# Performance work log

Hardware: AMD Instinct MI355X
Metric: run time of the kernel (lower is better)

The kernel has to match this reference:

```python
import jax, jax.numpy as jnp
import numpy as np
from math import ceil, log2

LEVELS = 6
N = 4096
DB4 = np.array([0.23037781330885523, 0.7148465705525415, 0.6308807679295904,
                -0.02798376941698385, -0.18703481171888114, 0.030841381835986965,
                0.032883011666982945, -0.010597401784997278], dtype=np.float32)


def setup_inputs() -> dict:
    key = jax.random.key(0)
    x = jax.random.normal(key, (N, N), dtype=jnp.float32)
    # learned filter bank: scaling.repeat(levels*2, 1)
    scaling = jnp.tile(jnp.asarray(DB4), (LEVELS * 2, 1))
    return {
        "x": x,
        "scaling": scaling,
        "alpha": jnp.float32(10.0),
        "b_plus": jnp.float32(2.0),
        "b_minus": jnp.float32(1.0),
    }


def compute_wavelet(h):
    # g_k = flip(h); odd indices negated
    g = jnp.flip(h, -1)
    sign = jnp.where(jnp.arange(g.shape[-1]) % 2 == 1, -1.0, 1.0).astype(g.dtype)
    return g * sign


def convolve(x, f, transpose=False):
    # circular convolution (or correlation if transpose) along last axis via FFT,
    # exactly as torch rfft/irfft with n=input_length
    L = x.shape[-1]
    fa = jnp.fft.rfft(x, axis=-1)
    fb = jnp.fft.rfft(f, n=L)
    if transpose:
        fb = jnp.conj(fb)
    return jnp.fft.irfft(fa * fb, n=L, axis=-1)


def forward_layer(x, h):
    w = compute_wavelet(h)
    return convolve(x, w)[:, ::2], convolve(x, h)[:, ::2]


def backward_layer(d, a, h):
    w = compute_wavelet(h)
    fd = jnp.zeros((d.shape[0], d.shape[1] * 2), d.dtype).at[:, ::2].set(d)
    fa = jnp.zeros((a.shape[0], a.shape[1] * 2), a.dtype).at[:, ::2].set(a)
    return convolve(fd, w, transpose=True) + convolve(fa, h, transpose=True)


def forward2d(x, hH, hV):
    d, a = forward_layer(x, hH)
    hh, hl = forward_layer(d.T, hV)
    hh, hl = hh.T, hl.T
    lh, ll = forward_layer(a.T, hV)
    lh, ll = lh.T, ll.T
    return (hh, hl, lh), ll


def backward2d(hh, hl, lh, ll, hH, hV):
    h = backward_layer(hh.T, hl.T, hV).T
    l = backward_layer(lh.T, ll.T, hV).T
    return backward_layer(h, l, hH)


def _despawn(x, scaling, alpha, b_plus, b_minus):
    n, m = x.shape
    pn = 2 ** ceil(log2(n)) - n
    pm = 2 ** ceil(log2(m)) - m
    xp = jnp.pad(x, ((0, pn), (0, pm)), mode="edge") if (pn or pm) else x

    approx = xp
    coeffs = []
    for lev in range(LEVELS):
        dets, approx = forward2d(approx, scaling[lev], scaling[lev + 1])
        coeffs.append(dets)

    def thr(t):
        return t * (jax.nn.sigmoid(alpha * (t - b_plus)) + jax.nn.sigmoid(-alpha * (t + b_minus)))

    filt = [tuple(thr(c) for c in tup) for tup in coeffs] + [thr(approx)]

    a = filt[-1]
    for lev in reversed(range(LEVELS)):
        hh, hl, lh = filt[lev]
        a = backward2d(hh, hl, lh, a, scaling[lev], scaling[lev + 1])

    flat = jnp.concatenate(
        [jnp.concatenate(tup, axis=-1).reshape(-1) for tup in filt[:-1]]
        + [filt[-1].reshape(-1)]
    )
    return a[:n, :m], flat


def reference(x, scaling, alpha, b_plus, b_minus):
    return _despawn(x, scaling, alpha, b_plus, b_minus)
```

## Files before the change

kernel.cpp:

```cpp
#include <hip/hip_runtime.h>


#define CORE_WGS 64

__device__ __forceinline__ float thrf(float t, float alpha, float bp, float bm) {
    float s1 = 1.0f / (1.0f + __expf(-alpha * (t - bp)));
    float s2 = 1.0f / (1.0f + __expf( alpha * (t + bm)));
    return t * (s1 + s2);
}

__device__ __forceinline__ void load_filt(const float* __restrict__ filt,
                                          float (&h)[8], float (&w)[8]) {
#pragma unroll
    for (int k = 0; k < 8; ++k) h[k] = filt[k];
#pragma unroll
    for (int k = 0; k < 8; ++k) w[k] = (k & 1) ? -h[7 - k] : h[7 - k];
}

struct SMemF {
    float xs[70][72];
    float Ds[70][36];
    float As[70][36];
};
struct SMemI {
    float hh[36][36], hl[36][36], lh[36][36], as0[36][36];
    float Hs[64][36], Ls[64][36];
};
union SMem {
    SMemF f;
    SMemI i;
};

__device__ __forceinline__ void gbar(unsigned* bar, unsigned k, unsigned nwg, int tid) {
    __syncthreads();
    if (tid == 0) {
        __threadfence();
        unsigned old = atomicAdd(&bar[0], 1u);
        if (old == k * nwg - 1u) {
            __hip_atomic_store(&bar[1], k, __ATOMIC_RELEASE, __HIP_MEMORY_SCOPE_AGENT);
            (void)__hip_atomic_load(&bar[1], __ATOMIC_ACQUIRE, __HIP_MEMORY_SCOPE_AGENT);
        } else {
            unsigned g;
            do {
                __builtin_amdgcn_s_sleep(2);
                g = __hip_atomic_load(&bar[1], __ATOMIC_ACQUIRE, __HIP_MEMORY_SCOPE_AGENT);
            } while (g < k);
        }
    }
    __syncthreads();
}

__device__ __forceinline__ void fwd_tile(
    SMemF& sm, const float* __restrict__ X, int s, int sh,
    float* __restrict__ flat, float* __restrict__ All, bool thr_ll,
    const float (&hr)[8], const float (&wr)[8],
    const float (&hc)[8], const float (&wc)[8],
    float alpha, float bp, float bm, int i0, int j0, int tid) {
    const int smk = s - 1;
    for (int idx = tid; idx < 70 * 18; idx += 256) {
        int rr = idx / 18, c = idx - rr * 18;
        int gr = (2 * i0 - 7 + rr) & smk;
        int gc = (2 * j0 - 8 + 4 * c) & smk;
        *(float4*)&sm.xs[rr][4 * c] = *(const float4*)&X[(size_t)gr * s + gc];
    }
    __syncthreads();
    for (int idx = tid; idx < 70 * 8; idx += 256) {
        int rr = idx >> 3, q = idx & 7;
        const float4* xr = (const float4*)&sm.xs[rr][8 * q];
        float wv[16];
#pragma unroll
        for (int m = 0; m < 4; ++m) {
            float4 t = xr[m];
            wv[4 * m + 0] = t.x; wv[4 * m + 1] = t.y;
            wv[4 * m + 2] = t.z; wv[4 * m + 3] = t.w;
        }
        float d[4], a[4];
#pragma unroll
        for (int e = 0; e < 4; ++e) {
            float dd = 0.f, aa = 0.f;
#pragma unroll
            for (int u = 0; u < 8; ++u) {
                float v = wv[2 * e + 1 + u];
                dd += wr[7 - u] * v;
                aa += hr[7 - u] * v;
            }
            d[e] = dd; a[e] = aa;
        }
        *(float4*)&sm.Ds[rr][4 * q] = make_float4(d[0], d[1], d[2], d[3]);
        *(float4*)&sm.As[rr][4 * q] = make_float4(a[0], a[1], a[2], a[3]);
    }
    __syncthreads();
    {
        const int j = tid & 31, iq = tid >> 5;
        float Dw[14], Aw[14];
#pragma unroll
        for (int t = 0; t < 14; ++t) {
            Dw[t] = sm.Ds[8 * iq + t][j];
            Aw[t] = sm.As[8 * iq + t][j];
        }
#pragma unroll
        for (int e = 0; e < 4; ++e) {
            float hh = 0.f, hl = 0.f, lh = 0.f, ll = 0.f;
#pragma unroll
            for (int u = 0; u < 8; ++u) {
                float dv = Dw[2 * e + u], av = Aw[2 * e + u];
                hh += wc[7 - u] * dv;
                hl += hc[7 - u] * dv;
                lh += wc[7 - u] * av;
                ll += hc[7 - u] * av;
            }
            int row = i0 + 4 * iq + e;
            size_t ro = (size_t)row * (3 * sh) + (j0 + j);
            flat[ro]          = thrf(hh, alpha, bp, bm);
            flat[ro + sh]     = thrf(hl, alpha, bp, bm);
            flat[ro + 2 * sh] = thrf(lh, alpha, bp, bm);
            All[(size_t)row * sh + (j0 + j)] =
                thr_ll ? thrf(ll, alpha, bp, bm) : ll;
        }
    }
}

__device__ __forceinline__ void inv_tile(
    SMemI& sm, const float* __restrict__ flatl, const float* __restrict__ a,
    int astride, int sc, float* __restrict__ outp, int ostride,
    const float (&hr)[8], const float (&wr)[8],
    const float (&hc)[8], const float (&wc)[8],
    int i0, int m0, int tid) {
    const int mm = sc - 1;
    const int r0 = i0 >> 1, c0 = m0 >> 1;
    const int ds = 3 * sc;
    for (int idx = tid; idx < 4 * 324; idx += 256) {
        int aid = idx / 324, rem = idx - aid * 324;
        int rr = rem / 9, c = rem - rr * 9;
        int gr = (r0 + rr) & mm;
        int gc = (c0 + 4 * c) & mm;
        if (aid == 0)
            *(float4*)&sm.hh[rr][4 * c] = *(const float4*)&flatl[(size_t)gr * ds + gc];
        else if (aid == 1)
            *(float4*)&sm.hl[rr][4 * c] = *(const float4*)&flatl[(size_t)gr * ds + sc + gc];
        else if (aid == 2)
            *(float4*)&sm.lh[rr][4 * c] = *(const float4*)&flatl[(size_t)gr * ds + 2 * sc + gc];
        else
            *(float4*)&sm.as0[rr][4 * c] = *(const float4*)&a[(size_t)gr * astride + gc];
    }
    __syncthreads();
    for (int idx = tid; idx < 16 * 36; idx += 256) {
        int q = idx / 36, jj = idx - q * 36;
        float hv[6], lv[6], gv[6], av[6];
#pragma unroll
        for (int d = 0; d < 6; ++d) {
            int lr = 2 * q + d;
            hv[d] = sm.hh[lr][jj];
            lv[d] = sm.hl[lr][jj];
            gv[d] = sm.lh[lr][jj];
            av[d] = sm.as0[lr][jj];
        }
        float H0 = 0.f, H1 = 0.f, H2 = 0.f, H3 = 0.f;
        float L0 = 0.f, L1 = 0.f, L2 = 0.f, L3 = 0.f;
#pragma unroll
        for (int t = 0; t < 4; ++t) {
            float we = wc[2 * t], he = hc[2 * t];
            float wo = wc[2 * t + 1], ho = hc[2 * t + 1];
            H0 += we * hv[t]     + he * lv[t];
            H1 += wo * hv[t + 1] + ho * lv[t + 1];
            H2 += we * hv[t + 1] + he * lv[t + 1];
            H3 += wo * hv[t + 2] + ho * lv[t + 2];
            L0 += we * gv[t]     + he * av[t];
            L1 += wo * gv[t + 1] + ho * av[t + 1];
            L2 += we * gv[t + 1] + he * av[t + 1];
            L3 += wo * gv[t + 2] + ho * av[t + 2];
        }
        sm.Hs[4 * q + 0][jj] = H0; sm.Hs[4 * q + 1][jj] = H1;
        sm.Hs[4 * q + 2][jj] = H2; sm.Hs[4 * q + 3][jj] = H3;
        sm.Ls[4 * q + 0][jj] = L0; sm.Ls[4 * q + 1][jj] = L1;
        sm.Ls[4 * q + 2][jj] = L2; sm.Ls[4 * q + 3][jj] = L3;
    }
    __syncthreads();
    for (int idx = tid; idx < 64 * 16; idx += 256) {
        int i = idx >> 4, p = idx & 15;
        const float2* hp = (const float2*)&sm.Hs[i][2 * p];
        const float2* lp = (const float2*)&sm.Ls[i][2 * p];
        float2 hA = hp[0], hB = hp[1], hC = hp[2];
        float2 lA = lp[0], lB = lp[1], lC = lp[2];
        float Hw[6] = {hA.x, hA.y, hB.x, hB.y, hC.x, hC.y};
        float Lw[6] = {lA.x, lA.y, lB.x, lB.y, lC.x, lC.y};
        float o0 = 0.f, o1 = 0.f, o2 = 0.f, o3 = 0.f;
#pragma unroll
        for (int t = 0; t < 4; ++t) {
            float we = wr[2 * t], he = hr[2 * t];
            float wo = wr[2 * t + 1], ho = hr[2 * t + 1];
            o0 += we * Hw[t]     + he * Lw[t];
            o1 += wo * Hw[t + 1] + ho * Lw[t + 1];
            o2 += we * Hw[t + 1] + he * Lw[t + 1];
            o3 += wo * Hw[t + 2] + ho * Lw[t + 2];
        }
        *(float4*)&outp[(size_t)(i0 + i) * ostride + (m0 + 4 * p)] =
            make_float4(o0, o1, o2, o3);
    }
}

__global__ __launch_bounds__(256) void fwd_fused(
    const float* __restrict__ X, int s, int sh,
    float* __restrict__ flat, float* __restrict__ All,
    const float* __restrict__ filt_row, const float* __restrict__ filt_col,
    const float* __restrict__ ap, const float* __restrict__ bpp,
    const float* __restrict__ bmp, unsigned* bar_reset) {
    __shared__ SMem smem;
    float hr[8], wr[8], hc[8], wc[8];
    load_filt(filt_row, hr, wr);
    load_filt(filt_col, hc, wc);
    const float alpha = *ap, bp = *bpp, bm = *bmp;
    fwd_tile(smem.f, X, s, sh, flat, All, false, hr, wr, hc, wc,
             alpha, bp, bm, blockIdx.y * 32, blockIdx.x * 32, threadIdx.x);
    if (bar_reset && blockIdx.x == 0 && blockIdx.y == 0 && threadIdx.x == 0) {
        bar_reset[0] = 0u;
        bar_reset[1] = 0u;
    }
}

__global__ __launch_bounds__(256) void inv_fused(
    const float* __restrict__ flatl, const float* __restrict__ a, int astride,
    int sc, float* __restrict__ outp, int ostride,
    const float* __restrict__ filt_col, const float* __restrict__ filt_row) {
    __shared__ SMem smem;
    float hr[8], wr[8], hc[8], wc[8];
    load_filt(filt_row, hr, wr);
    load_filt(filt_col, hc, wc);
    inv_tile(smem.i, flatl, a, astride, sc, outp, ostride, hr, wr, hc, wc,
             blockIdx.y * 64, blockIdx.x * 64, threadIdx.x);
}

__global__ __launch_bounds__(256) void core_small(
    const float* __restrict__ scal, const float* __restrict__ ap,
    const float* __restrict__ bpp, const float* __restrict__ bmp,
    float* __restrict__ out, float* __restrict__ ws, unsigned* bar) {
    __shared__ SMem smem;
    const int tid = threadIdx.x, bid = blockIdx.x, nb = gridDim.x;
    const float alpha = *ap, bp = *bpp, bm = *bmp;
    const int N = 4096;
    float* flat = out + 16777216;
    const size_t Aoff[7]    = {0, 0, 4194304, 5242880, 5505024, 5570560, 5586944};
    const size_t flatOff[6] = {0, 12582912, 15728640, 16515072, 16711680, 16760832};
    const size_t finalOff = 16773120;
    float* P0 = ws + 5591040;
    float* P1 = ws + 5591040 + 4194304;

    unsigned k = 1;
    for (int lev = 3; lev <= 5; ++lev) {
        int s = N >> lev, sh = s >> 1;
        float hr[8], wr[8], hc[8], wc[8];
        load_filt(scal + lev * 8, hr, wr);
        load_filt(scal + (lev + 1) * 8, hc, wc);
        const float* src = ws + Aoff[lev];
        float* All = (lev < 5) ? (ws + Aoff[lev + 1]) : (flat + finalOff);
        int nt = sh >> 5;
        for (int t = bid; t < nt * nt; t += nb)
            fwd_tile(smem.f, src, s, sh, flat + flatOff[lev], All, lev == 5,
                     hr, wr, hc, wc, alpha, bp, bm, (t / nt) * 32, (t % nt) * 32, tid);
        gbar(bar, k++, (unsigned)nb, tid);
    }
    const float* a_in = flat + finalOff;
    for (int lev = 5; lev >= 3; --lev) {
        int sc = N >> (lev + 1), r = 2 * sc;
        float hr[8], wr[8], hc[8], wc[8];
        load_filt(scal + lev * 8, hr, wr);
        load_filt(scal + (lev + 1) * 8, hc, wc);
        float* outp = (lev & 1) ? P1 : P0;
        int nt = r >> 6;
        for (int t = bid; t < nt * nt; t += nb)
            inv_tile(smem.i, flat + flatOff[lev], a_in, sc, sc, outp, r,
                     hr, wr, hc, wc, (t / nt) * 64, (t % nt) * 64, tid);
        a_in = outp;
        if (lev > 3) gbar(bar, k++, (unsigned)nb, tid);
    }
}

extern "C" void kernel_launch(void* const* d_in, const int* in_sizes, int n_in,
                              void* d_out, int out_size, void* d_ws, size_t ws_size,
                              hipStream_t stream) {
    const float* x    = (const float*)d_in[0];
    const float* scal = (const float*)d_in[1];
    const float* ap   = (const float*)d_in[2];
    const float* bp   = (const float*)d_in[3];
    const float* bm   = (const float*)d_in[4];
    float* out = (float*)d_out;
    float* ws  = (float*)d_ws;

    const int N = 4096;
    float* recon = out;
    float* flat  = out + 16777216;
    static const size_t Aoff[7]    = {0, 0, 4194304, 5242880, 5505024, 5570560, 5586944};
    static const size_t flatOff[6] = {0, 12582912, 15728640, 16515072, 16711680, 16760832};
    float* P0 = ws + 5591040;
    float* P1 = ws + 5591040 + 4194304;
    unsigned* bar = (unsigned*)(ws + 14680064);

    dim3 blk(256);

    const float* src = x;
    for (int lev = 0; lev < 3; ++lev) {
        int s = N >> lev, sh = s >> 1;
        dim3 g(sh / 32, sh / 32);
        fwd_fused<<<g, blk, 0, stream>>>(src, s, sh, flat + flatOff[lev],
                                         ws + Aoff[lev + 1],
                                         scal + lev * 8, scal + (lev + 1) * 8,
                                         ap, bp, bm,
                                         (lev == 2) ? bar : (unsigned*)nullptr);
        src = ws + Aoff[lev + 1];
    }

    {
        void* args[] = {(void*)&scal, (void*)&ap, (void*)&bp, (void*)&bm,
                        (void*)&out, (void*)&ws, (void*)&bar};
        hipLaunchCooperativeKernel(core_small, dim3(CORE_WGS), blk, args, 0, stream);
    }

    const float* a_in = P1;
    for (int lev = 2; lev >= 0; --lev) {
        int sc = N >> (lev + 1), r = 2 * sc;
        float* outp = (lev == 0) ? recon : ((lev & 1) ? P1 : P0);
        dim3 g(r / 64, r / 64);
        inv_fused<<<g, blk, 0, stream>>>(flat + flatOff[lev], a_in, sc,
                                         sc, outp, r,
                                         scal + (lev + 1) * 8, scal + lev * 8);
        a_in = outp;
    }
}
```

Baseline: 349.4 us.

## Replace grid barrier with per-phase tile counters and launch core kernel normally

The persistent core kernel's generic grid barrier is replaced by per-phase completion counters, each on its own padded cache line. A block waits only until the previous phase's tile count is reached, and blocks with no tiles skip signalling. The cooperative launch is replaced by a plain launch to cut launch overhead. This relies on all 64 workgroups being co-resident without the cooperative guarantee, and adds extra __syncthreads between tiles in each loop.

```diff
diff --git a/kernel.cpp b/kernel.cpp
--- a/kernel.cpp
+++ b/kernel.cpp
@@ -30,25 +30,6 @@
     SMemF f;
     SMemI i;
 };
-
-__device__ __forceinline__ void gbar(unsigned* bar, unsigned k, unsigned nwg, int tid) {
-    __syncthreads();
-    if (tid == 0) {
-        __threadfence();
-        unsigned old = atomicAdd(&bar[0], 1u);
-        if (old == k * nwg - 1u) {
-            __hip_atomic_store(&bar[1], k, __ATOMIC_RELEASE, __HIP_MEMORY_SCOPE_AGENT);
-            (void)__hip_atomic_load(&bar[1], __ATOMIC_ACQUIRE, __HIP_MEMORY_SCOPE_AGENT);
-        } else {
-            unsigned g;
-            do {
-                __builtin_amdgcn_s_sleep(2);
-                g = __hip_atomic_load(&bar[1], __ATOMIC_ACQUIRE, __HIP_MEMORY_SCOPE_AGENT);
-            } while (g < k);
-        }
-    }
-    __syncthreads();
-}
 
 __device__ __forceinline__ void fwd_tile(
     SMemF& sm, const float* __restrict__ X, int s, int sh,
@@ -212,10 +193,8 @@
     const float alpha = *ap, bp = *bpp, bm = *bmp;
     fwd_tile(smem.f, X, s, sh, flat, All, false, hr, wr, hc, wc,
              alpha, bp, bm, blockIdx.y * 32, blockIdx.x * 32, threadIdx.x);
-    if (bar_reset && blockIdx.x == 0 && blockIdx.y == 0 && threadIdx.x == 0) {
-        bar_reset[0] = 0u;
-        bar_reset[1] = 0u;
-    }
+    if (bar_reset && blockIdx.x == 0 && blockIdx.y == 0 && threadIdx.x < 8)
+        bar_reset[threadIdx.x * 32] = 0u;
 }
 
 __global__ __launch_bounds__(256) void inv_fused(
@@ -233,7 +212,7 @@
 __global__ __launch_bounds__(256) void core_small(
     const float* __restrict__ scal, const float* __restrict__ ap,
     const float* __restrict__ bpp, const float* __restrict__ bmp,
-    float* __restrict__ out, float* __restrict__ ws, unsigned* bar) {
+    float* __restrict__ out, float* __restrict__ ws, unsigned* __restrict__ bar) {
     __shared__ SMem smem;
     const int tid = threadIdx.x, bid = blockIdx.x, nb = gridDim.x;
     const float alpha = *ap, bp = *bpp, bm = *bmp;
@@ -245,33 +224,59 @@
     float* P0 = ws + 5591040;
     float* P1 = ws + 5591040 + 4194304;
 
-    unsigned k = 1;
-    for (int lev = 3; lev <= 5; ++lev) {
-        int s = N >> lev, sh = s >> 1;
+    const float* a_in = flat + finalOff;
+    for (int p = 0; p < 6; ++p) {
+        const int lev = (p < 3) ? (3 + p) : (8 - p);
+        const int nt  = N >> (lev + 6);
+        const int Np  = nt * nt;
+
+        if (p > 0) {
+            const int pl  = (p - 1 < 3) ? (2 + p) : (9 - p);
+            const int pnt = N >> (pl + 6);
+            const unsigned tgt = (unsigned)(pnt * pnt);
+            if (tid == 0) {
+                while (__hip_atomic_load(&bar[(p - 1) * 32], __ATOMIC_RELAXED,
+                                         __HIP_MEMORY_SCOPE_AGENT) < tgt) {
+                    __builtin_amdgcn_s_sleep(2);
+                }
+            }
+            __syncthreads();
+            __builtin_amdgcn_fence(__ATOMIC_ACQUIRE, "agent");
+        }
+
         float hr[8], wr[8], hc[8], wc[8];
         load_filt(scal + lev * 8, hr, wr);
         load_filt(scal + (lev + 1) * 8, hc, wc);
-        const float* src = ws + Aoff[lev];
-        float* All = (lev < 5) ? (ws + Aoff[lev + 1]) : (flat + finalOff);
-        int nt = sh >> 5;
-        for (int t = bid; t < nt * nt; t += nb)
-            fwd_tile(smem.f, src, s, sh, flat + flatOff[lev], All, lev == 5,
-                     hr, wr, hc, wc, alpha, bp, bm, (t / nt) * 32, (t % nt) * 32, tid);
-        gbar(bar, k++, (unsigned)nb, tid);
-    }
-    const float* a_in = flat + finalOff;
-    for (int lev = 5; lev >= 3; --lev) {
-        int sc = N >> (lev + 1), r = 2 * sc;
-        float hr[8], wr[8], hc[8], wc[8];
-        load_filt(scal + lev * 8, hr, wr);
-        load_filt(scal + (lev + 1) * 8, hc, wc);
-        float* outp = (lev & 1) ? P1 : P0;
-        int nt = r >> 6;
-        for (int t = bid; t < nt * nt; t += nb)
-            inv_tile(smem.i, flat + flatOff[lev], a_in, sc, sc, outp, r,
-                     hr, wr, hc, wc, (t / nt) * 64, (t % nt) * 64, tid);
-        a_in = outp;
-        if (lev > 3) gbar(bar, k++, (unsigned)nb, tid);
+        unsigned cnt = 0;
+
+        if (p < 3) {
+            const int s = N >> lev, sh = s >> 1;
+            const float* src = ws + Aoff[lev];
+            float* All = (lev < 5) ? (ws + Aoff[lev + 1]) : (flat + finalOff);
+            for (int t = bid; t < Np; t += nb) {
+                if (cnt) __syncthreads();
+                fwd_tile(smem.f, src, s, sh, flat + flatOff[lev], All, lev == 5,
+                         hr, wr, hc, wc, alpha, bp, bm,
+                         (t / nt) * 32, (t % nt) * 32, tid);
+                ++cnt;
+            }
+        } else {
+            const int sc = N >> (lev + 1), r = 2 * sc;
+            float* outp = (lev & 1) ? P1 : P0;
+            for (int t = bid; t < Np; t += nb) {
+                if (cnt) __syncthreads();
+                inv_tile(smem.i, flat + flatOff[lev], a_in, sc, sc, outp, r,
+                         hr, wr, hc, wc, (t / nt) * 64, (t % nt) * 64, tid);
+                ++cnt;
+            }
+            a_in = outp;
+        }
+
+        __syncthreads();
+        if (tid == 0 && cnt) {
+            __threadfence();
+            atomicAdd(&bar[p * 32], cnt);
+        }
     }
 }
 
@@ -309,11 +314,7 @@
         src = ws + Aoff[lev + 1];
     }
 
-    {
-        void* args[] = {(void*)&scal, (void*)&ap, (void*)&bp, (void*)&bm,
-                        (void*)&out, (void*)&ws, (void*)&bar};
-        hipLaunchCooperativeKernel(core_small, dim3(CORE_WGS), blk, args, 0, stream);
-    }
+    core_small<<<dim3(CORE_WGS), blk, 0, stream>>>(scal, ap, bp, bm, out, ws, bar);
 
     const float* a_in = P1;
     for (int lev = 2; lev >= 0; --lev) {
```

Result: faster. 321.2 us (-8.1%).
